# Performance work log

Hardware: AMD Instinct MI355X
Metric: run time of the kernel (lower is better)

The kernel has to match this reference:

```python
import jax, jax.numpy as jnp
import numpy as np

B, S, M = 8, 2048, 256
D = 512          # input/memory feature dim
P = 512          # proj_dim
H = 8            # num_heads


def setup_inputs() -> dict:
    key = jax.random.key(0)
    ks = jax.random.split(key, 10)
    sc = 0.02
    return {
        "input_seq": jax.random.normal(ks[0], (B, S, D), jnp.float32),
        "memory_cells": jax.random.normal(ks[1], (B, M, D), jnp.float32),
        "Wk": jax.random.normal(ks[2], (D, P), jnp.float32) * sc,
        "bk": jnp.zeros((P,), jnp.float32),
        "Wv": jax.random.normal(ks[3], (D, P), jnp.float32) * sc,
        "bv": jnp.zeros((P,), jnp.float32),
        "Wq": jax.random.normal(ks[4], (H, D, P), jnp.float32) * sc,  # stacked per-head query Dense
        "bq": jnp.zeros((H, P), jnp.float32),
        "Wo": jax.random.normal(ks[5], (H * P, P), jnp.float32) * sc,
        "bo": jnp.zeros((P,), jnp.float32),
    }


def reference(input_seq, memory_cells, Wk, bk, Wv, bv, Wq, bq, Wo, bo):
    # shared key/value projections (multi-query: one K/V for all heads)
    ik = input_seq @ Wk + bk          # [B,S,P]
    mk = memory_cells @ Wk + bk       # [B,M,P]
    iv = input_seq @ Wv + bv          # [B,S,P]
    mv = memory_cells @ Wv + bv       # [B,M,P]

    # per-head queries from memory cells, all heads at once
    q = jnp.einsum('bmd,hdp->bhmp', memory_cells, Wq) + bq[None, :, None, :]  # [B,H,M,P]

    input_score = jnp.einsum('bhmp,bsp->bhms', q, ik)          # [B,H,M,S]
    self_score = jnp.sum(q * mk[:, None], axis=-1, keepdims=True)  # [B,H,M,1]
    score = jnp.concatenate([self_score, input_score], axis=-1)    # [B,H,M,S+1]
    score = score / jnp.sqrt(jnp.float32(P))
    attn = jax.nn.softmax(score, axis=-1)

    self_attn = attn[..., 0:1]                                  # [B,H,M,1]
    input_attn = attn[..., 1:]                                  # [B,H,M,S]
    val = jnp.einsum('bhms,bsp->bhmp', input_attn, iv) + self_attn * mv[:, None]

    # concat heads: [B,M,H*P]
    concat = jnp.transpose(val, (0, 2, 1, 3)).reshape(B, M, H * P)
    return concat @ Wo + bo           # [B,M,P]
```

## Files before the change

kernel.cpp:

```cpp
#include <hip/hip_runtime.h>

#define B_ 8
#define S_ 2048
#define M_ 256
#define D_ 512
#define P_ 512
#define H_ 8

#define SCALE 0.044194173824159216f

typedef __attribute__((ext_vector_type(8))) short bf16x8;
typedef __attribute__((ext_vector_type(4))) float f32x4;

static __device__ __forceinline__ float bf2f(short u) {
  union { float f; unsigned int i; } x;
  x.i = ((unsigned int)(unsigned short)u) << 16;
  return x.f;
}
static __device__ __forceinline__ short f2bf(float f) {
  union { float f; unsigned int i; } x;
  x.f = f;
  unsigned int r = (x.i + 0x7FFFu + ((x.i >> 16) & 1u)) >> 16;
  return (short)r;
}

static __device__ __forceinline__ void gll16(const short* g, short* l) {
  __builtin_amdgcn_global_load_lds(
      (const __attribute__((address_space(1))) void*)g,
      (__attribute__((address_space(3))) void*)l, 16, 0, 0);
}

#define LGKM_WAIT() asm volatile("s_waitcnt lgkmcnt(0)" ::: "memory")
#define RAW_BAR() do { asm volatile("" ::: "memory"); __builtin_amdgcn_s_barrier(); asm volatile("" ::: "memory"); } while (0)

__global__ __launch_bounds__(256) void cast_both(
    const float* __restrict__ inA, short* __restrict__ outA, int n4A,
    const float* __restrict__ inM, short* __restrict__ outM)
{
  int idx = blockIdx.x * 256 + threadIdx.x;
  const float* in = inA;
  short* out = outA;
  if (idx >= n4A) { idx -= n4A; in = inM; out = outM; }
  float4 v = ((const float4*)in)[idx];
  short o0 = f2bf(v.x), o1 = f2bf(v.y), o2 = f2bf(v.z), o3 = f2bf(v.w);
  uint2 pk;
  pk.x = (unsigned int)(unsigned short)o0 | ((unsigned int)(unsigned short)o1 << 16);
  pk.y = (unsigned int)(unsigned short)o2 | ((unsigned int)(unsigned short)o3 << 16);
  ((uint2*)out)[idx] = pk;
}

__global__ __launch_bounds__(256) void wtrans_all(
    const float* __restrict__ Wk, const float* __restrict__ Wv,
    const float* __restrict__ Wq,
    short* __restrict__ WkT, short* __restrict__ WvT, short* __restrict__ WqT)
{
  __shared__ float tile[32][33];
  const int t = threadIdx.x, tx = t & 31, ty = t >> 5;
  const int z = blockIdx.z;
  const float* inp;
  short* outp;
  if (z == 0)      { inp = Wk; outp = WkT; }
  else if (z == 1) { inp = Wv; outp = WvT; }
  else             { inp = Wq + (size_t)(z - 2) * 512 * 512;
                     outp = WqT + (size_t)(z - 2) * 512 * 512; }
  const int n0 = blockIdx.x * 32, k0 = blockIdx.y * 32;
#pragma unroll
  for (int i = 0; i < 4; ++i)
    tile[ty + 8 * i][tx] = inp[(size_t)(k0 + ty + 8 * i) * 512 + n0 + tx];
  __syncthreads();
#pragma unroll
  for (int i = 0; i < 4; ++i)
    outp[(size_t)(n0 + ty + 8 * i) * 512 + k0 + tx] = f2bf(tile[tx][ty + 8 * i]);
}

__global__ __launch_bounds__(256) void wtrans_wo(
    const float* __restrict__ in, short* __restrict__ out)
{
  __shared__ float tile[32][33];
  const int t = threadIdx.x, tx = t & 31, ty = t >> 5;
  const int n0 = blockIdx.x * 32, k0 = blockIdx.y * 32;
#pragma unroll
  for (int i = 0; i < 4; ++i)
    tile[ty + 8 * i][tx] = in[(size_t)(k0 + ty + 8 * i) * 512 + n0 + tx];
  __syncthreads();
#pragma unroll
  for (int i = 0; i < 4; ++i)
    out[(size_t)(n0 + ty + 8 * i) * 4096 + k0 + tx] = f2bf(tile[tx][ty + 8 * i]);
}

template<int MODE, int K, int N, int LDA, int LDB>
__global__ __launch_bounds__(256, 3) void gemm128(
    const short* __restrict__ Abase, const short* __restrict__ Bbase,
    const float* __restrict__ bias, void* __restrict__ Cv,
    const size_t aZ, const size_t bZ, const size_t cZ,
    float* __restrict__ Ls,
    const float* __restrict__ eselfp, const short* __restrict__ mvbp)
{
  __shared__ short As[4096];
  __shared__ short Bs[4096];
  const int t = threadIdx.x;
  const int w = t >> 6, lane = t & 63, qd = lane >> 4, ln = lane & 15;
  const int wm = (w & 1) * 64, wn = (w >> 1) * 64;

  int z, m0, n0, bsel;
  if constexpr (MODE == 2 || MODE == 3) {
    const int b = blockIdx.x;
    n0 = blockIdx.y * 128;
    const int h = blockIdx.z & 7, mb = blockIdx.z >> 3;
    z = b * 8 + h;
    m0 = mb * 128;
    bsel = b;
  } else {
    n0 = blockIdx.x * 128;
    m0 = blockIdx.y * 128;
    z = blockIdx.z;
    bsel = z;
  }

  const short* A  = Abase + (size_t)z * aZ;
  const short* Bp = Bbase + (size_t)bsel * bZ;

  const int rr = t >> 2, g0 = t & 3;
  const int gs0 = g0 ^ ((rr >> 1) & 3);
  const int gs1 = g0 ^ (((rr + 64) >> 1) & 3);
  const short* ga0 = A + (size_t)(m0 + rr) * LDA + gs0 * 8;
  const short* ga1 = A + (size_t)(m0 + rr + 64) * LDA + gs1 * 8;
  const short* gb0 = Bp + (size_t)(n0 + rr) * LDB + gs0 * 8;
  const short* gb1 = Bp + (size_t)(n0 + rr + 64) * LDB + gs1 * 8;

  int aoff[4], boff[4];
#pragma unroll
  for (int mt = 0; mt < 4; ++mt) {
    int r = wm + mt * 16 + ln;
    aoff[mt] = r * 32 + (qd ^ ((r >> 1) & 3)) * 8;
  }
#pragma unroll
  for (int nt = 0; nt < 4; ++nt) {
    int r = wn + nt * 16 + ln;
    boff[nt] = r * 32 + (qd ^ ((r >> 1) & 3)) * 8;
  }

  f32x4 acc[4][4];
#pragma unroll
  for (int mt = 0; mt < 4; ++mt)
#pragma unroll
    for (int nt = 0; nt < 4; ++nt) acc[mt][nt] = (f32x4){0.f, 0.f, 0.f, 0.f};

  for (int kc = 0; kc < K; kc += 32) {
    __syncthreads();
    gll16(ga0 + kc, &As[w * 512]);
    gll16(ga1 + kc, &As[2048 + w * 512]);
    gll16(gb0 + kc, &Bs[w * 512]);
    gll16(gb1 + kc, &Bs[2048 + w * 512]);
    __syncthreads();

    bf16x8 af[4], bfr[4];
#pragma unroll
    for (int mt = 0; mt < 4; ++mt) af[mt] = *(const bf16x8*)&As[aoff[mt]];
#pragma unroll
    for (int nt = 0; nt < 4; ++nt) bfr[nt] = *(const bf16x8*)&Bs[boff[nt]];
#pragma unroll
    for (int mt = 0; mt < 4; ++mt)
#pragma unroll
      for (int nt = 0; nt < 4; ++nt)
        acc[mt][nt] = __builtin_amdgcn_mfma_f32_16x16x32_bf16(af[mt], bfr[nt], acc[mt][nt], 0, 0, 0);
  }

  if constexpr (MODE == 5) {
#pragma unroll
    for (int nt = 0; nt < 4; ++nt) {
      const int col = n0 + wn + nt * 16 + ln;
#pragma unroll
      for (int mt = 0; mt < 4; ++mt)
#pragma unroll
        for (int r = 0; r < 4; ++r) {
          const int row = m0 + wm + mt * 16 + qd * 4 + r;
          ((float*)Cv)[(size_t)z * cZ + (size_t)row * N + col] = acc[mt][nt][r];
        }
    }
  } else if constexpr (MODE == 2) {
#pragma unroll
    for (int mt = 0; mt < 4; ++mt)
#pragma unroll
      for (int nt = 0; nt < 4; ++nt)
#pragma unroll
        for (int r = 0; r < 4; ++r)
          acc[mt][nt][r] = __expf(acc[mt][nt][r] * SCALE);
#pragma unroll
    for (int mt = 0; mt < 4; ++mt)
#pragma unroll
      for (int r = 0; r < 4; ++r) {
        float rsum = acc[mt][0][r] + acc[mt][1][r] + acc[mt][2][r] + acc[mt][3][r];
        rsum += __shfl_xor(rsum, 1);
        rsum += __shfl_xor(rsum, 2);
        rsum += __shfl_xor(rsum, 4);
        rsum += __shfl_xor(rsum, 8);
        if (ln == 0) {
          const int row = m0 + wm + mt * 16 + qd * 4 + r;
          atomicAdd(&Ls[(size_t)z * M_ + row], rsum);
        }
      }
#pragma unroll
    for (int nt = 0; nt < 4; ++nt) {
      const int col = n0 + wn + nt * 16 + ln;
#pragma unroll
      for (int mt = 0; mt < 4; ++mt)
#pragma unroll
        for (int r = 0; r < 4; ++r) {
          const int row = m0 + wm + mt * 16 + qd * 4 + r;
          ((short*)Cv)[(size_t)z * cZ + (size_t)row * N + col] = f2bf(acc[mt][nt][r]);
        }
    }
  } else if constexpr (MODE == 3) {
    const int zb = z >> 3, hh = z & 7;
#pragma unroll
    for (int mt = 0; mt < 4; ++mt)
#pragma unroll
      for (int r = 0; r < 4; ++r) {
        const int row = m0 + wm + mt * 16 + qd * 4 + r;
        const float es = eselfp[(size_t)z * M_ + row];
        const float inv = 1.f / (es + Ls[(size_t)z * M_ + row]);
        const short* mvr = mvbp + ((size_t)(zb * M_ + row)) * P_;
        short* outr = (short*)Cv + ((size_t)(zb * M_ + row)) * (H_ * P_) + (size_t)hh * P_;
#pragma unroll
        for (int nt = 0; nt < 4; ++nt) {
          const int col = n0 + wn + nt * 16 + ln;
          outr[col] = f2bf((acc[mt][nt][r] + es * bf2f(mvr[col])) * inv);
        }
      }
  } else {
#pragma unroll
    for (int nt = 0; nt < 4; ++nt) {
      const int col = n0 + wn + nt * 16 + ln;
      const float bc = bias[512 * z + col];
#pragma unroll
      for (int mt = 0; mt < 4; ++mt)
#pragma unroll
        for (int r = 0; r < 4; ++r) {
          const int row = m0 + wm + mt * 16 + qd * 4 + r;
          const int bidx = row >> 8, ml = row & 255;
          ((short*)Cv)[((size_t)(bidx * H_ + z) * M_ + ml) * N + col] = f2bf(acc[mt][nt][r] + bc);
        }
    }
  }
}

template<int MH, int NH>
static __device__ __forceinline__ void mfma_quad(
    f32x4 (&acc)[8][4], const bf16x8 (&a)[4][2], const bf16x8 (&bfr)[2][2])
{
  __builtin_amdgcn_s_setprio(1);
#pragma unroll
  for (int kk = 0; kk < 2; ++kk)
#pragma unroll
    for (int mt = 0; mt < 4; ++mt)
#pragma unroll
      for (int nt = 0; nt < 2; ++nt)
        acc[MH * 4 + mt][NH * 2 + nt] = __builtin_amdgcn_mfma_f32_16x16x32_bf16(
            a[mt][kk], bfr[nt][kk], acc[MH * 4 + mt][NH * 2 + nt], 0, 0, 0);
  __builtin_amdgcn_s_setprio(0);
}

template<int MODE, int K, int LDA, int LDB>
__global__ __launch_bounds__(512, 2) void gemm256(
    const short* __restrict__ Abase, const short* __restrict__ Bbase,
    void* __restrict__ Cv, float* __restrict__ Ls,
    const float* __restrict__ eselfp, const short* __restrict__ mvbp,
    const size_t aZ, const size_t bZ)
{
  __shared__ short lds[65536];
  constexpr int NKT = K / 64;
  static_assert(NKT >= 2, "need at least 2 K-tiles");
  const int t = threadIdx.x;
  const int w = t >> 6, lane = t & 63, qd = lane >> 4, ln = lane & 15;
  const int wr = w >> 2, wc = w & 3;
  const int b = blockIdx.x;
  const int n0 = blockIdx.y * 256, m0 = blockIdx.z * 256;

  const short* A  = Abase + (size_t)b * aZ;
  const short* Bp = Bbase + (size_t)b * bZ;

  const int s0 = w * 64 + lane, s1 = s0 + 512;
  const int sr0 = s0 >> 3, sc0 = ((s0 & 7) ^ (sr0 & 7)) * 8;
  const int sr1 = s1 >> 3, sc1 = ((s1 & 7) ^ (sr1 & 7)) * 8;

  auto stage = [&](const short* gorigin, int ldg, short* lbase) {
    gll16(gorigin + (size_t)sr0 * ldg + sc0, lbase + w * 512);
    gll16(gorigin + (size_t)sr1 * ldg + sc1, lbase + 4096 + w * 512);
  };

  const int cq0 = ((qd    ) ^ (ln & 7)) * 8;
  const int cq1 = ((4 + qd) ^ (ln & 7)) * 8;
  const int brow = (wc & 1) * 64;

  f32x4 acc[8][4];
#pragma unroll
  for (int i = 0; i < 8; ++i)
#pragma unroll
    for (int j = 0; j < 4; ++j) acc[i][j] = (f32x4){0.f, 0.f, 0.f, 0.f};

  stage(A  + (size_t)m0 * LDA,          LDA, &lds[0]);
  stage(A  + (size_t)(m0 + 128) * LDA,  LDA, &lds[8192]);
  stage(Bp + (size_t)n0 * LDB,          LDB, &lds[32768]);
  stage(Bp + (size_t)(n0 + 128) * LDB,  LDB, &lds[32768 + 8192]);
  stage(Bp + (size_t)n0 * LDB + 64,     LDB, &lds[32768 + 16384]);
  asm volatile("s_waitcnt vmcnt(2)" ::: "memory");
  __builtin_amdgcn_s_barrier();

#pragma unroll 1
  for (int kt = 0; kt < NKT; ++kt) {
    const int p = kt & 1;
    short* Ah = &lds[p * 16384 + wr * 8192];
    short* Bh = &lds[32768 + p * 16384 + (wc >> 1) * 8192];
    bf16x8 a[4][2], bfr[2][2];

#pragma unroll
    for (int mt = 0; mt < 4; ++mt) {
      a[mt][0] = *(const bf16x8*)&Ah[(mt * 16 + ln) * 64 + cq0];
      a[mt][1] = *(const bf16x8*)&Ah[(mt * 16 + ln) * 64 + cq1];
    }
#pragma unroll
    for (int nt = 0; nt < 2; ++nt) {
      bfr[nt][0] = *(const bf16x8*)&Bh[(brow + nt * 16 + ln) * 64 + cq0];
      bfr[nt][1] = *(const bf16x8*)&Bh[(brow + nt * 16 + ln) * 64 + cq1];
    }
    if (kt + 1 < NKT) {
      stage(A  + (size_t)m0 * LDA + (kt + 1) * 64,          LDA, &lds[(p ^ 1) * 16384]);
      stage(Bp + (size_t)(n0 + 128) * LDB + (kt + 1) * 64,  LDB, &lds[32768 + (p ^ 1) * 16384 + 8192]);
    }
    RAW_BAR(); LGKM_WAIT();
    mfma_quad<0, 0>(acc, a, bfr);
    RAW_BAR();

#pragma unroll
    for (int mt = 0; mt < 4; ++mt) {
      a[mt][0] = *(const bf16x8*)&Ah[4096 + (mt * 16 + ln) * 64 + cq0];
      a[mt][1] = *(const bf16x8*)&Ah[4096 + (mt * 16 + ln) * 64 + cq1];
    }
    if (kt + 1 < NKT)
      stage(A + (size_t)(m0 + 128) * LDA + (kt + 1) * 64, LDA, &lds[(p ^ 1) * 16384 + 8192]);
    RAW_BAR(); LGKM_WAIT();
    mfma_quad<1, 0>(acc, a, bfr);
    RAW_BAR();

#pragma unroll
    for (int nt = 0; nt < 2; ++nt) {
      bfr[nt][0] = *(const bf16x8*)&Bh[(brow + 32 + nt * 16 + ln) * 64 + cq0];
      bfr[nt][1] = *(const bf16x8*)&Bh[(brow + 32 + nt * 16 + ln) * 64 + cq1];
    }
    RAW_BAR(); LGKM_WAIT();
    mfma_quad<1, 1>(acc, a, bfr);
    RAW_BAR();

#pragma unroll
    for (int mt = 0; mt < 4; ++mt) {
      a[mt][0] = *(const bf16x8*)&Ah[(mt * 16 + ln) * 64 + cq0];
      a[mt][1] = *(const bf16x8*)&Ah[(mt * 16 + ln) * 64 + cq1];
    }
    if (kt + 2 < NKT)
      stage(Bp + (size_t)n0 * LDB + (kt + 2) * 64, LDB, &lds[32768 + p * 16384]);
    RAW_BAR(); LGKM_WAIT();
    mfma_quad<0, 1>(acc, a, bfr);
    if (kt + 2 < NKT) { asm volatile("s_waitcnt vmcnt(2)" ::: "memory"); }
    else              { asm volatile("s_waitcnt vmcnt(0)" ::: "memory"); }
    RAW_BAR();
  }

  if constexpr (MODE == 2) {
#pragma unroll
    for (int i = 0; i < 8; ++i)
#pragma unroll
      for (int j = 0; j < 4; ++j)
#pragma unroll
        for (int r = 0; r < 4; ++r)
          acc[i][j][r] = __expf(acc[i][j][r] * SCALE);
#pragma unroll
    for (int i = 0; i < 8; ++i)
#pragma unroll
      for (int r = 0; r < 4; ++r) {
        float rs = acc[i][0][r] + acc[i][1][r] + acc[i][2][r] + acc[i][3][r];
        rs += __shfl_xor(rs, 1);
        rs += __shfl_xor(rs, 2);
        rs += __shfl_xor(rs, 4);
        rs += __shfl_xor(rs, 8);
        if (ln == 0) {
          const int row = m0 + wr * 128 + i * 16 + qd * 4 + r;
          atomicAdd(&Ls[(size_t)b * 2048 + row], rs);
        }
      }
    short* Cb = (short*)Cv + (size_t)b * 2048 * 2048;
#pragma unroll
    for (int j = 0; j < 4; ++j) {
      const int col = n0 + wc * 64 + j * 16 + ln;
#pragma unroll
      for (int i = 0; i < 8; ++i)
#pragma unroll
        for (int r = 0; r < 4; ++r) {
          const int row = m0 + wr * 128 + i * 16 + qd * 4 + r;
          Cb[(size_t)row * 2048 + col] = f2bf(acc[i][j][r]);
        }
    }
  } else {
#pragma unroll
    for (int i = 0; i < 8; ++i)
#pragma unroll
      for (int r = 0; r < 4; ++r) {
        const int R = m0 + wr * 128 + i * 16 + qd * 4 + r;
        const float es  = eselfp[(size_t)b * 2048 + R];
        const float inv = 1.f / (es + Ls[(size_t)b * 2048 + R]);
        const int h = R >> 8, m = R & 255;
        const short* mvr = mvbp + ((size_t)(b * 256 + m)) * 512;
        short* outr = (short*)Cv + ((size_t)(b * 256 + m)) * 4096 + (size_t)h * 512;
#pragma unroll
        for (int j = 0; j < 4; ++j) {
          const int col = n0 + wc * 64 + j * 16 + ln;
          outr[col] = f2bf((acc[i][j][r] + es * bf2f(mvr[col])) * inv);
        }
      }
  }
}

template<bool TRANSV>
__global__ __launch_bounds__(256, 3) void proj_kv(
    const short* __restrict__ A,
    const short* __restrict__ WkT, const short* __restrict__ WvT,
    const float* __restrict__ bk, const float* __restrict__ bv,
    short* __restrict__ Ck, short* __restrict__ Cvv)
{
  __shared__ short Sh[8192];
  short* As  = Sh;
  short* Bks = Sh + 4096;
  short* Bvs = Sh + 6144;
  const int t = threadIdx.x;
  const int w = t >> 6, lane = t & 63, qd = lane >> 4, ln = lane & 15;
  const int n0 = blockIdx.x * 64, m0 = blockIdx.y * 128;
  const int wm = (w & 1) * 64, wn2 = (w >> 1) * 32;

  const int rr = t >> 2, g0 = t & 3;
  const int gs0 = g0 ^ ((rr >> 1) & 3);
  const int gs1 = g0 ^ (((rr + 64) >> 1) & 3);
  const short* ga0 = A + (size_t)(m0 + rr) * 512 + gs0 * 8;
  const short* ga1 = A + (size_t)(m0 + rr + 64) * 512 + gs1 * 8;
  const short* gbk = WkT + (size_t)(n0 + rr) * 512 + gs0 * 8;
  const short* gbv = WvT + (size_t)(n0 + rr) * 512 + gs0 * 8;

  int aoff[4], boff[2];
#pragma unroll
  for (int mt = 0; mt < 4; ++mt) {
    int r = wm + mt * 16 + ln;
    aoff[mt] = r * 32 + (qd ^ ((r >> 1) & 3)) * 8;
  }
#pragma unroll
  for (int nt = 0; nt < 2; ++nt) {
    int r = wn2 + nt * 16 + ln;
    boff[nt] = r * 32 + (qd ^ ((r >> 1) & 3)) * 8;
  }

  f32x4 accK[4][2], accV[4][2];
#pragma unroll
  for (int mt = 0; mt < 4; ++mt)
#pragma unroll
    for (int nt = 0; nt < 2; ++nt) {
      accK[mt][nt] = (f32x4){0.f, 0.f, 0.f, 0.f};
      accV[mt][nt] = (f32x4){0.f, 0.f, 0.f, 0.f};
    }

  for (int kc = 0; kc < 512; kc += 32) {
    __syncthreads();
    gll16(ga0 + kc, &As[w * 512]);
    gll16(ga1 + kc, &As[2048 + w * 512]);
    gll16(gbk + kc, &Bks[w * 512]);
    gll16(gbv + kc, &Bvs[w * 512]);
    __syncthreads();

    bf16x8 af[4], bkf[2], bvf[2];
#pragma unroll
    for (int mt = 0; mt < 4; ++mt) af[mt] = *(const bf16x8*)&As[aoff[mt]];
#pragma unroll
    for (int nt = 0; nt < 2; ++nt) {
      bkf[nt] = *(const bf16x8*)&Bks[boff[nt]];
      bvf[nt] = *(const bf16x8*)&Bvs[boff[nt]];
    }
#pragma unroll
    for (int mt = 0; mt < 4; ++mt)
#pragma unroll
      for (int nt = 0; nt < 2; ++nt) {
        accK[mt][nt] = __builtin_amdgcn_mfma_f32_16x16x32_bf16(af[mt], bkf[nt], accK[mt][nt], 0, 0, 0);
        accV[mt][nt] = __builtin_amdgcn_mfma_f32_16x16x32_bf16(af[mt], bvf[nt], accV[mt][nt], 0, 0, 0);
      }
  }

#pragma unroll
  for (int nt = 0; nt < 2; ++nt) {
    const int col = n0 + wn2 + nt * 16 + ln;
    const float bc = bk[col];
#pragma unroll
    for (int mt = 0; mt < 4; ++mt)
#pragma unroll
      for (int r = 0; r < 4; ++r) {
        const int row = m0 + wm + mt * 16 + qd * 4 + r;
        Ck[(size_t)row * 512 + col] = f2bf(accK[mt][nt][r] + bc);
      }
  }

  if constexpr (!TRANSV) {
#pragma unroll
    for (int nt = 0; nt < 2; ++nt) {
      const int col = n0 + wn2 + nt * 16 + ln;
      const float bc = bv[col];
#pragma unroll
      for (int mt = 0; mt < 4; ++mt)
#pragma unroll
        for (int r = 0; r < 4; ++r) {
          const int row = m0 + wm + mt * 16 + qd * 4 + r;
          Cvv[(size_t)row * 512 + col] = f2bf(accV[mt][nt][r] + bc);
        }
    }
  } else {
    __syncthreads();
    short* ep = &Sh[w * 1280];
    const int lr = lane >> 1, lc16 = (lane & 1) * 16;
#pragma unroll
    for (int pass = 0; pass < 2; ++pass) {
#pragma unroll
      for (int mh = 0; mh < 2; ++mh) {
        const int mt = pass * 2 + mh;
#pragma unroll
        for (int nt = 0; nt < 2; ++nt) {
          const float bc = bv[n0 + wn2 + nt * 16 + ln];
#pragma unroll
          for (int r = 0; r < 4; ++r)
            ep[(nt * 16 + ln) * 40 + mh * 16 + qd * 4 + r] = f2bf(accV[mt][nt][r] + bc);
        }
      }
      LGKM_WAIT();
      const int srow0 = m0 + wm + pass * 32;
      const int bidx = srow0 >> 11;
      const int sloc = (srow0 & 2047) + lc16;
      const int pcol = n0 + wn2 + lr;
      short* outp = Cvv + (size_t)bidx * P_ * S_ + (size_t)pcol * S_ + sloc;
      *(bf16x8*)outp = *(const bf16x8*)&ep[lr * 40 + lc16];
      *(bf16x8*)(outp + 8) = *(const bf16x8*)&ep[lr * 40 + lc16 + 8];
      LGKM_WAIT();
    }
  }
}

__global__ __launch_bounds__(256) void reduce_wo(
    const float* __restrict__ partial, const float* __restrict__ bo,
    float* __restrict__ out)
{
  const int idx4 = blockIdx.x * 256 + threadIdx.x;
  float4 s = ((const float4*)bo)[idx4 & 127];
#pragma unroll
  for (int zz = 0; zz < 4; ++zz) {
    float4 p = ((const float4*)partial)[(size_t)zz * 262144 + idx4];
    s.x += p.x; s.y += p.y; s.z += p.z; s.w += p.w;
  }
  ((float4*)out)[idx4] = s;
}

__global__ __launch_bounds__(256) void selfscore(
    const short* __restrict__ qb, const short* __restrict__ mkb,
    float* __restrict__ eself, float* __restrict__ Ls)
{
  const int z = blockIdx.x, t = threadIdx.x;
  const short* qr = qb + ((size_t)z * M_ + t) * P_;
  const short* mr = mkb + ((size_t)(z >> 3) * M_ + t) * P_;
  float s = 0.f;
#pragma unroll 8
  for (int c = 0; c < P_; c += 8) {
    bf16x8 qv = *(const bf16x8*)(qr + c);
    bf16x8 mv = *(const bf16x8*)(mr + c);
#pragma unroll
    for (int j = 0; j < 8; ++j) s += bf2f(qv[j]) * bf2f(mv[j]);
  }
  eself[(size_t)z * M_ + t] = __expf(s * SCALE);
  Ls[(size_t)z * M_ + t] = 0.f;
}

extern "C" void kernel_launch(void* const* d_in, const int* in_sizes, int n_in,
                              void* d_out, int out_size, void* d_ws, size_t ws_size,
                              hipStream_t stream) {
  const float* input_seq = (const float*)d_in[0];
  const float* memcells  = (const float*)d_in[1];
  const float* Wk = (const float*)d_in[2];
  const float* bk = (const float*)d_in[3];
  const float* Wv = (const float*)d_in[4];
  const float* bv = (const float*)d_in[5];
  const float* Wq = (const float*)d_in[6];
  const float* bq = (const float*)d_in[7];
  const float* Wo = (const float*)d_in[8];
  const float* bo = (const float*)d_in[9];
  float* out = (float*)d_out;

  short* ws = (short*)d_ws;
  size_t o = 0;
  short* valb = ws + o; o += (size_t)B_ * M_ * H_ * P_;
  short* WoT  = ws + o; o += (size_t)(H_ * P_) * P_;
  short* mvb  = ws + o; o += (size_t)B_ * M_ * P_;
  short* mkb  = ws + o; o += (size_t)B_ * M_ * P_;
  short* qb   = ws + o; o += (size_t)B_ * H_ * M_ * P_;
  short* ivT  = ws + o; o += (size_t)B_ * P_ * S_;
  short* ikb  = ws + o; o += (size_t)B_ * S_ * P_;
  float* partial = (float*)(ws + o); o += (size_t)B_ * H_ * M_ * P_;
  float* eself = (float*)(ws + o); o += 2 * (size_t)B_ * H_ * M_;
  float* Ls    = (float*)(ws + o); o += 2 * (size_t)B_ * H_ * M_;
  short* region2 = ws + o;
  short* Ab  = region2;
  short* Mb  = Ab + (size_t)B_ * S_ * D_;
  short* WkT = Mb + (size_t)B_ * M_ * D_;
  short* WvT = WkT + (size_t)D_ * P_;
  short* WqT = WvT + (size_t)D_ * P_;
  short* Eb  = region2;

  dim3 blk(256);

  const int n4A = B_ * S_ * D_ / 4;
  const int n4M = B_ * M_ * D_ / 4;
  cast_both<<<dim3((n4A + n4M) / 256), blk, 0, stream>>>(input_seq, Ab, n4A, memcells, Mb);
  wtrans_all<<<dim3(16, 16, 10), blk, 0, stream>>>(Wk, Wv, Wq, WkT, WvT, WqT);
  wtrans_wo<<<dim3(16, 128), blk, 0, stream>>>(Wo, WoT);

  proj_kv<true><<<dim3(8, 128), blk, 0, stream>>>(Ab, WkT, WvT, bk, bv, ikb, ivT);
  proj_kv<false><<<dim3(8, 16), blk, 0, stream>>>(Mb, WkT, WvT, bk, bv, mkb, mvb);

  gemm128<1, 512, 512, 512, 512><<<dim3(4, 16, 8), blk, 0, stream>>>(
      Mb, WqT, bq, qb, 0, (size_t)D_ * P_, 0, nullptr, nullptr, nullptr);

  selfscore<<<dim3(64), blk, 0, stream>>>(qb, mkb, eself, Ls);

  gemm256<2, 512, 512, 512><<<dim3(8, 8, 8), dim3(512), 0, stream>>>(
      qb, ikb, Eb, Ls, nullptr, nullptr,
      (size_t)2048 * 512, (size_t)2048 * 512);

  gemm256<3, 2048, 2048, 2048><<<dim3(8, 2, 8), dim3(512), 0, stream>>>(
      Eb, ivT, valb, Ls, eself, mvb,
      (size_t)2048 * 2048, (size_t)512 * 2048);

  gemm128<5, 1024, 512, 4096, 4096><<<dim3(4, 16, 4), blk, 0, stream>>>(
      valb, WoT, nullptr, partial, 1024, 1024,
      (size_t)2048 * 512, nullptr, nullptr, nullptr);
  reduce_wo<<<dim3(1024), blk, 0, stream>>>(partial, bo, out);
}
```

Baseline: 325.3 us.

## Split attention GEMMs into qk256 and pv128 kernels with LDS-staged coalesced stores

Replaces the templated gemm256 with two kernels. qk256 reorders its global-to-LDS staging and MFMA phases, and writes the exp-score tile back through LDS so global stores are 16-byte and coalesced. pv128 narrows the N tile to 128, which doubles the grid from 128 to 256 blocks so the CUs fill better, and it also stages its normalized output through LDS for wide stores. It also drops the unused MODE 2/3 paths from gemm128 and adds a sched_barrier after the LDS waits. The cost is extra LDS traffic in the epilogues, and the narrower P·V tile reuses each A tile less.

```diff
diff --git a/kernel.cpp b/kernel.cpp
--- a/kernel.cpp
+++ b/kernel.cpp
@@ -31,6 +31,8 @@
 }
 
 #define LGKM_WAIT() asm volatile("s_waitcnt lgkmcnt(0)" ::: "memory")
+#define LGKM_SYNC() do { asm volatile("s_waitcnt lgkmcnt(0)" ::: "memory"); \
+                         __builtin_amdgcn_sched_barrier(0); } while (0)
 #define RAW_BAR() do { asm volatile("" ::: "memory"); __builtin_amdgcn_s_barrier(); asm volatile("" ::: "memory"); } while (0)
 
 __global__ __launch_bounds__(256) void cast_both(
@@ -102,20 +104,10 @@
   const int w = t >> 6, lane = t & 63, qd = lane >> 4, ln = lane & 15;
   const int wm = (w & 1) * 64, wn = (w >> 1) * 64;
 
-  int z, m0, n0, bsel;
-  if constexpr (MODE == 2 || MODE == 3) {
-    const int b = blockIdx.x;
-    n0 = blockIdx.y * 128;
-    const int h = blockIdx.z & 7, mb = blockIdx.z >> 3;
-    z = b * 8 + h;
-    m0 = mb * 128;
-    bsel = b;
-  } else {
-    n0 = blockIdx.x * 128;
-    m0 = blockIdx.y * 128;
-    z = blockIdx.z;
-    bsel = z;
-  }
+  const int n0 = blockIdx.x * 128;
+  const int m0 = blockIdx.y * 128;
+  const int z = blockIdx.z;
+  const int bsel = z;
 
   const short* A  = Abase + (size_t)z * aZ;
   const short* Bp = Bbase + (size_t)bsel * bZ;
@@ -178,56 +170,6 @@
           ((float*)Cv)[(size_t)z * cZ + (size_t)row * N + col] = acc[mt][nt][r];
         }
     }
-  } else if constexpr (MODE == 2) {
-#pragma unroll
-    for (int mt = 0; mt < 4; ++mt)
-#pragma unroll
-      for (int nt = 0; nt < 4; ++nt)
-#pragma unroll
-        for (int r = 0; r < 4; ++r)
-          acc[mt][nt][r] = __expf(acc[mt][nt][r] * SCALE);
-#pragma unroll
-    for (int mt = 0; mt < 4; ++mt)
-#pragma unroll
-      for (int r = 0; r < 4; ++r) {
-        float rsum = acc[mt][0][r] + acc[mt][1][r] + acc[mt][2][r] + acc[mt][3][r];
-        rsum += __shfl_xor(rsum, 1);
-        rsum += __shfl_xor(rsum, 2);
-        rsum += __shfl_xor(rsum, 4);
-        rsum += __shfl_xor(rsum, 8);
-        if (ln == 0) {
-          const int row = m0 + wm + mt * 16 + qd * 4 + r;
-          atomicAdd(&Ls[(size_t)z * M_ + row], rsum);
-        }
-      }
-#pragma unroll
-    for (int nt = 0; nt < 4; ++nt) {
-      const int col = n0 + wn + nt * 16 + ln;
-#pragma unroll
-      for (int mt = 0; mt < 4; ++mt)
-#pragma unroll
-        for (int r = 0; r < 4; ++r) {
-          const int row = m0 + wm + mt * 16 + qd * 4 + r;
-          ((short*)Cv)[(size_t)z * cZ + (size_t)row * N + col] = f2bf(acc[mt][nt][r]);
-        }
-    }
-  } else if constexpr (MODE == 3) {
-    const int zb = z >> 3, hh = z & 7;
-#pragma unroll
-    for (int mt = 0; mt < 4; ++mt)
-#pragma unroll
-      for (int r = 0; r < 4; ++r) {
-        const int row = m0 + wm + mt * 16 + qd * 4 + r;
-        const float es = eselfp[(size_t)z * M_ + row];
-        const float inv = 1.f / (es + Ls[(size_t)z * M_ + row]);
-        const short* mvr = mvbp + ((size_t)(zb * M_ + row)) * P_;
-        short* outr = (short*)Cv + ((size_t)(zb * M_ + row)) * (H_ * P_) + (size_t)hh * P_;
-#pragma unroll
-        for (int nt = 0; nt < 4; ++nt) {
-          const int col = n0 + wn + nt * 16 + ln;
-          outr[col] = f2bf((acc[mt][nt][r] + es * bf2f(mvr[col])) * inv);
-        }
-      }
   } else {
 #pragma unroll
     for (int nt = 0; nt < 4; ++nt) {
@@ -261,32 +203,41 @@
   __builtin_amdgcn_s_setprio(0);
 }
 
-template<int MODE, int K, int LDA, int LDB>
-__global__ __launch_bounds__(512, 2) void gemm256(
+template<int MH, int NT>
+static __device__ __forceinline__ void mfma_oct(
+    f32x4 (&acc)[8][2], const bf16x8 (&a)[4][2], const bf16x8 (&bv)[2])
+{
+  __builtin_amdgcn_s_setprio(1);
+#pragma unroll
+  for (int kk = 0; kk < 2; ++kk)
+#pragma unroll
+    for (int mt = 0; mt < 4; ++mt)
+      acc[MH * 4 + mt][NT] = __builtin_amdgcn_mfma_f32_16x16x32_bf16(
+          a[mt][kk], bv[kk], acc[MH * 4 + mt][NT], 0, 0, 0);
+  __builtin_amdgcn_s_setprio(0);
+}
+
+template<int NKT>
+__global__ __launch_bounds__(512, 2) void qk256(
     const short* __restrict__ Abase, const short* __restrict__ Bbase,
-    void* __restrict__ Cv, float* __restrict__ Ls,
-    const float* __restrict__ eselfp, const short* __restrict__ mvbp,
-    const size_t aZ, const size_t bZ)
+    short* __restrict__ Eb, float* __restrict__ Ls)
 {
   __shared__ short lds[65536];
-  constexpr int NKT = K / 64;
-  static_assert(NKT >= 2, "need at least 2 K-tiles");
   const int t = threadIdx.x;
   const int w = t >> 6, lane = t & 63, qd = lane >> 4, ln = lane & 15;
   const int wr = w >> 2, wc = w & 3;
   const int b = blockIdx.x;
   const int n0 = blockIdx.y * 256, m0 = blockIdx.z * 256;
 
-  const short* A  = Abase + (size_t)b * aZ;
-  const short* Bp = Bbase + (size_t)b * bZ;
+  const short* A  = Abase + (size_t)b * (2048 * 512) + (size_t)m0 * 512;
+  const short* Bp = Bbase + (size_t)b * (2048 * 512) + (size_t)n0 * 512;
 
   const int s0 = w * 64 + lane, s1 = s0 + 512;
   const int sr0 = s0 >> 3, sc0 = ((s0 & 7) ^ (sr0 & 7)) * 8;
   const int sr1 = s1 >> 3, sc1 = ((s1 & 7) ^ (sr1 & 7)) * 8;
-
-  auto stage = [&](const short* gorigin, int ldg, short* lbase) {
-    gll16(gorigin + (size_t)sr0 * ldg + sc0, lbase + w * 512);
-    gll16(gorigin + (size_t)sr1 * ldg + sc1, lbase + 4096 + w * 512);
+  auto stage = [&](const short* g, short* lbase) {
+    gll16(g + (size_t)sr0 * 512 + sc0, lbase + w * 512);
+    gll16(g + (size_t)sr1 * 512 + sc1, lbase + 4096 + w * 512);
   };
 
   const int cq0 = ((qd    ) ^ (ln & 7)) * 8;
@@ -299,12 +250,13 @@
 #pragma unroll
     for (int j = 0; j < 4; ++j) acc[i][j] = (f32x4){0.f, 0.f, 0.f, 0.f};
 
-  stage(A  + (size_t)m0 * LDA,          LDA, &lds[0]);
-  stage(A  + (size_t)(m0 + 128) * LDA,  LDA, &lds[8192]);
-  stage(Bp + (size_t)n0 * LDB,          LDB, &lds[32768]);
-  stage(Bp + (size_t)(n0 + 128) * LDB,  LDB, &lds[32768 + 8192]);
-  stage(Bp + (size_t)n0 * LDB + 64,     LDB, &lds[32768 + 16384]);
-  asm volatile("s_waitcnt vmcnt(2)" ::: "memory");
+  stage(A,                  &lds[0]);
+  stage(A + 128 * 512,      &lds[8192]);
+  stage(Bp,                 &lds[32768]);
+  stage(Bp + 128 * 512,     &lds[32768 + 8192]);
+  stage(A + 64,             &lds[16384]);
+  stage(A + 128 * 512 + 64, &lds[16384 + 8192]);
+  asm volatile("s_waitcnt vmcnt(4)" ::: "memory");
   __builtin_amdgcn_s_barrier();
 
 #pragma unroll 1
@@ -325,11 +277,20 @@
       bfr[nt][1] = *(const bf16x8*)&Bh[(brow + nt * 16 + ln) * 64 + cq1];
     }
     if (kt + 1 < NKT) {
-      stage(A  + (size_t)m0 * LDA + (kt + 1) * 64,          LDA, &lds[(p ^ 1) * 16384]);
-      stage(Bp + (size_t)(n0 + 128) * LDB + (kt + 1) * 64,  LDB, &lds[32768 + (p ^ 1) * 16384 + 8192]);
-    }
-    RAW_BAR(); LGKM_WAIT();
+      stage(Bp + (kt + 1) * 64,             &lds[32768 + (p ^ 1) * 16384]);
+      stage(Bp + 128 * 512 + (kt + 1) * 64, &lds[32768 + (p ^ 1) * 16384 + 8192]);
+    }
+    RAW_BAR(); LGKM_SYNC();
     mfma_quad<0, 0>(acc, a, bfr);
+    RAW_BAR();
+
+#pragma unroll
+    for (int nt = 0; nt < 2; ++nt) {
+      bfr[nt][0] = *(const bf16x8*)&Bh[(brow + 32 + nt * 16 + ln) * 64 + cq0];
+      bfr[nt][1] = *(const bf16x8*)&Bh[(brow + 32 + nt * 16 + ln) * 64 + cq1];
+    }
+    RAW_BAR(); LGKM_SYNC();
+    mfma_quad<0, 1>(acc, a, bfr);
     RAW_BAR();
 
 #pragma unroll
@@ -337,86 +298,184 @@
       a[mt][0] = *(const bf16x8*)&Ah[4096 + (mt * 16 + ln) * 64 + cq0];
       a[mt][1] = *(const bf16x8*)&Ah[4096 + (mt * 16 + ln) * 64 + cq1];
     }
-    if (kt + 1 < NKT)
-      stage(A + (size_t)(m0 + 128) * LDA + (kt + 1) * 64, LDA, &lds[(p ^ 1) * 16384 + 8192]);
-    RAW_BAR(); LGKM_WAIT();
-    mfma_quad<1, 0>(acc, a, bfr);
-    RAW_BAR();
-
-#pragma unroll
-    for (int nt = 0; nt < 2; ++nt) {
-      bfr[nt][0] = *(const bf16x8*)&Bh[(brow + 32 + nt * 16 + ln) * 64 + cq0];
-      bfr[nt][1] = *(const bf16x8*)&Bh[(brow + 32 + nt * 16 + ln) * 64 + cq1];
-    }
-    RAW_BAR(); LGKM_WAIT();
+    RAW_BAR(); LGKM_SYNC();
     mfma_quad<1, 1>(acc, a, bfr);
     RAW_BAR();
+
+#pragma unroll
+    for (int nt = 0; nt < 2; ++nt) {
+      bfr[nt][0] = *(const bf16x8*)&Bh[(brow + nt * 16 + ln) * 64 + cq0];
+      bfr[nt][1] = *(const bf16x8*)&Bh[(brow + nt * 16 + ln) * 64 + cq1];
+    }
+    if (kt + 2 < NKT) {
+      stage(A + (kt + 2) * 64,             &lds[p * 16384]);
+      stage(A + 128 * 512 + (kt + 2) * 64, &lds[p * 16384 + 8192]);
+    }
+    RAW_BAR(); LGKM_SYNC();
+    mfma_quad<1, 0>(acc, a, bfr);
+    if (kt + 2 < NKT) { asm volatile("s_waitcnt vmcnt(4)" ::: "memory"); }
+    else              { asm volatile("s_waitcnt vmcnt(0)" ::: "memory"); }
+    RAW_BAR();
+  }
+
+#pragma unroll
+  for (int i = 0; i < 8; ++i)
+#pragma unroll
+    for (int j = 0; j < 4; ++j)
+#pragma unroll
+      for (int r = 0; r < 4; ++r)
+        acc[i][j][r] = __expf(acc[i][j][r] * SCALE);
+#pragma unroll
+  for (int i = 0; i < 8; ++i)
+#pragma unroll
+    for (int r = 0; r < 4; ++r) {
+      float rs = acc[i][0][r] + acc[i][1][r] + acc[i][2][r] + acc[i][3][r];
+      rs += __shfl_xor(rs, 1);
+      rs += __shfl_xor(rs, 2);
+      rs += __shfl_xor(rs, 4);
+      rs += __shfl_xor(rs, 8);
+      if (ln == 0) {
+        const int row = m0 + wr * 128 + i * 16 + qd * 4 + r;
+        atomicAdd(&Ls[(size_t)b * 2048 + row], rs);
+      }
+    }
+#pragma unroll
+  for (int i = 0; i < 8; ++i)
+#pragma unroll
+    for (int j = 0; j < 4; ++j)
+#pragma unroll
+      for (int r = 0; r < 4; ++r) {
+        const int row = wr * 128 + i * 16 + qd * 4 + r;
+        const int col = wc * 64 + j * 16 + ln;
+        lds[row * 256 + (col ^ ((row & 7) << 3))] = f2bf(acc[i][j][r]);
+      }
+  LGKM_WAIT();
+  RAW_BAR();
+  short* Cb = Eb + (size_t)b * 2048 * 2048;
+#pragma unroll
+  for (int it = 0; it < 16; ++it) {
+    const int flat = it * 512 + t;
+    const int row = flat >> 5, c = flat & 31;
+    bf16x8 v = *(const bf16x8*)&lds[row * 256 + ((c ^ (row & 7)) * 8)];
+    *(bf16x8*)(Cb + (size_t)(m0 + row) * 2048 + n0 + c * 8) = v;
+  }
+}
+
+template<int NKT>
+__global__ __launch_bounds__(512, 2) void pv128(
+    const short* __restrict__ Abase, const short* __restrict__ Bbase,
+    short* __restrict__ valb, const float* __restrict__ Ls,
+    const float* __restrict__ eselfp, const short* __restrict__ mvbp)
+{
+  __shared__ short lds[49152];
+  const int t = threadIdx.x;
+  const int w = t >> 6, lane = t & 63, qd = lane >> 4, ln = lane & 15;
+  const int wr = w >> 2, wc = w & 3;
+  const int b = blockIdx.x;
+  const int n0 = blockIdx.y * 128;
+  const int bz = blockIdx.z;
+  const int m0 = bz * 256;
+
+  const short* A  = Abase + (size_t)b * (2048 * 2048) + (size_t)m0 * 2048;
+  const short* Bp = Bbase + (size_t)b * (512 * 2048) + (size_t)n0 * 2048;
+
+  const int s0 = w * 64 + lane, s1 = s0 + 512;
+  const int sr0 = s0 >> 3, sc0 = ((s0 & 7) ^ (sr0 & 7)) * 8;
+  const int sr1 = s1 >> 3, sc1 = ((s1 & 7) ^ (sr1 & 7)) * 8;
+  auto stage = [&](const short* g, short* lbase) {
+    gll16(g + (size_t)sr0 * 2048 + sc0, lbase + w * 512);
+    gll16(g + (size_t)sr1 * 2048 + sc1, lbase + 4096 + w * 512);
+  };
+
+  const int cq0 = ((qd    ) ^ (ln & 7)) * 8;
+  const int cq1 = ((4 + qd) ^ (ln & 7)) * 8;
+  const int brow = wc * 32;
+
+  f32x4 acc[8][2];
+#pragma unroll
+  for (int i = 0; i < 8; ++i)
+#pragma unroll
+    for (int j = 0; j < 2; ++j) acc[i][j] = (f32x4){0.f, 0.f, 0.f, 0.f};
+
+  stage(A,                   &lds[0]);
+  stage(A + 128 * 2048,      &lds[8192]);
+  stage(Bp,                  &lds[32768]);
+  stage(A + 64,              &lds[16384]);
+  stage(A + 128 * 2048 + 64, &lds[16384 + 8192]);
+  asm volatile("s_waitcnt vmcnt(4)" ::: "memory");
+  __builtin_amdgcn_s_barrier();
+
+#pragma unroll 1
+  for (int kt = 0; kt < NKT; ++kt) {
+    const int p = kt & 1;
+    short* Ah = &lds[p * 16384 + wr * 8192];
+    short* Bh = &lds[32768 + p * 8192];
+    bf16x8 a[4][2], bv[2];
 
 #pragma unroll
     for (int mt = 0; mt < 4; ++mt) {
       a[mt][0] = *(const bf16x8*)&Ah[(mt * 16 + ln) * 64 + cq0];
       a[mt][1] = *(const bf16x8*)&Ah[(mt * 16 + ln) * 64 + cq1];
     }
-    if (kt + 2 < NKT)
-      stage(Bp + (size_t)n0 * LDB + (kt + 2) * 64, LDB, &lds[32768 + p * 16384]);
-    RAW_BAR(); LGKM_WAIT();
-    mfma_quad<0, 1>(acc, a, bfr);
-    if (kt + 2 < NKT) { asm volatile("s_waitcnt vmcnt(2)" ::: "memory"); }
+    bv[0] = *(const bf16x8*)&Bh[(brow + ln) * 64 + cq0];
+    bv[1] = *(const bf16x8*)&Bh[(brow + ln) * 64 + cq1];
+    if (kt + 1 < NKT)
+      stage(Bp + (kt + 1) * 64, &lds[32768 + (p ^ 1) * 8192]);
+    RAW_BAR(); LGKM_SYNC();
+    mfma_oct<0, 0>(acc, a, bv);
+    RAW_BAR();
+
+    bv[0] = *(const bf16x8*)&Bh[(brow + 16 + ln) * 64 + cq0];
+    bv[1] = *(const bf16x8*)&Bh[(brow + 16 + ln) * 64 + cq1];
+    RAW_BAR(); LGKM_SYNC();
+    mfma_oct<0, 1>(acc, a, bv);
+    RAW_BAR();
+
+#pragma unroll
+    for (int mt = 0; mt < 4; ++mt) {
+      a[mt][0] = *(const bf16x8*)&Ah[4096 + (mt * 16 + ln) * 64 + cq0];
+      a[mt][1] = *(const bf16x8*)&Ah[4096 + (mt * 16 + ln) * 64 + cq1];
+    }
+    RAW_BAR(); LGKM_SYNC();
+    mfma_oct<1, 1>(acc, a, bv);
+    RAW_BAR();
+
+    bv[0] = *(const bf16x8*)&Bh[(brow + ln) * 64 + cq0];
+    bv[1] = *(const bf16x8*)&Bh[(brow + ln) * 64 + cq1];
+    if (kt + 2 < NKT) {
+      stage(A + (kt + 2) * 64,              &lds[p * 16384]);
+      stage(A + 128 * 2048 + (kt + 2) * 64, &lds[p * 16384 + 8192]);
+    }
+    RAW_BAR(); LGKM_SYNC();
+    mfma_oct<1, 0>(acc, a, bv);
+    if (kt + 2 < NKT) { asm volatile("s_waitcnt vmcnt(4)" ::: "memory"); }
     else              { asm volatile("s_waitcnt vmcnt(0)" ::: "memory"); }
     RAW_BAR();
   }
 
-  if constexpr (MODE == 2) {
-#pragma unroll
-    for (int i = 0; i < 8; ++i)
-#pragma unroll
-      for (int j = 0; j < 4; ++j)
-#pragma unroll
-        for (int r = 0; r < 4; ++r)
-          acc[i][j][r] = __expf(acc[i][j][r] * SCALE);
-#pragma unroll
-    for (int i = 0; i < 8; ++i)
-#pragma unroll
-      for (int r = 0; r < 4; ++r) {
-        float rs = acc[i][0][r] + acc[i][1][r] + acc[i][2][r] + acc[i][3][r];
-        rs += __shfl_xor(rs, 1);
-        rs += __shfl_xor(rs, 2);
-        rs += __shfl_xor(rs, 4);
-        rs += __shfl_xor(rs, 8);
-        if (ln == 0) {
-          const int row = m0 + wr * 128 + i * 16 + qd * 4 + r;
-          atomicAdd(&Ls[(size_t)b * 2048 + row], rs);
-        }
+#pragma unroll
+  for (int i = 0; i < 8; ++i)
+#pragma unroll
+    for (int r = 0; r < 4; ++r) {
+      const int row = wr * 128 + i * 16 + qd * 4 + r;
+      const float es  = eselfp[(size_t)b * 2048 + m0 + row];
+      const float inv = 1.f / (es + Ls[(size_t)b * 2048 + m0 + row]);
+      const short* mvr = mvbp + ((size_t)(b * 256 + row)) * 512;
+#pragma unroll
+      for (int j = 0; j < 2; ++j) {
+        const int lcol = wc * 32 + j * 16 + ln;
+        const float v = (acc[i][j][r] + es * bf2f(mvr[n0 + lcol])) * inv;
+        lds[row * 128 + (lcol ^ ((row & 7) << 3))] = f2bf(v);
       }
-    short* Cb = (short*)Cv + (size_t)b * 2048 * 2048;
-#pragma unroll
-    for (int j = 0; j < 4; ++j) {
-      const int col = n0 + wc * 64 + j * 16 + ln;
-#pragma unroll
-      for (int i = 0; i < 8; ++i)
-#pragma unroll
-        for (int r = 0; r < 4; ++r) {
-          const int row = m0 + wr * 128 + i * 16 + qd * 4 + r;
-          Cb[(size_t)row * 2048 + col] = f2bf(acc[i][j][r]);
-        }
-    }
-  } else {
-#pragma unroll
-    for (int i = 0; i < 8; ++i)
-#pragma unroll
-      for (int r = 0; r < 4; ++r) {
-        const int R = m0 + wr * 128 + i * 16 + qd * 4 + r;
-        const float es  = eselfp[(size_t)b * 2048 + R];
-        const float inv = 1.f / (es + Ls[(size_t)b * 2048 + R]);
-        const int h = R >> 8, m = R & 255;
-        const short* mvr = mvbp + ((size_t)(b * 256 + m)) * 512;
-        short* outr = (short*)Cv + ((size_t)(b * 256 + m)) * 4096 + (size_t)h * 512;
-#pragma unroll
-        for (int j = 0; j < 4; ++j) {
-          const int col = n0 + wc * 64 + j * 16 + ln;
-          outr[col] = f2bf((acc[i][j][r] + es * bf2f(mvr[col])) * inv);
-        }
-      }
+    }
+  LGKM_WAIT();
+  RAW_BAR();
+#pragma unroll
+  for (int it = 0; it < 8; ++it) {
+    const int flat = it * 512 + t;
+    const int row = flat >> 4, c = flat & 15;
+    bf16x8 v = *(const bf16x8*)&lds[row * 128 + ((c ^ (row & 7)) * 8)];
+    *(bf16x8*)(valb + ((size_t)(b * 256 + row)) * 4096 + (size_t)bz * 512 + n0 + c * 8) = v;
   }
 }
 
@@ -630,13 +689,9 @@
 
   selfscore<<<dim3(64), blk, 0, stream>>>(qb, mkb, eself, Ls);
 
-  gemm256<2, 512, 512, 512><<<dim3(8, 8, 8), dim3(512), 0, stream>>>(
-      qb, ikb, Eb, Ls, nullptr, nullptr,
-      (size_t)2048 * 512, (size_t)2048 * 512);
-
-  gemm256<3, 2048, 2048, 2048><<<dim3(8, 2, 8), dim3(512), 0, stream>>>(
-      Eb, ivT, valb, Ls, eself, mvb,
-      (size_t)2048 * 2048, (size_t)512 * 2048);
+  qk256<8><<<dim3(8, 8, 8), dim3(512), 0, stream>>>(qb, ikb, Eb, Ls);
+
+  pv128<32><<<dim3(8, 4, 8), dim3(512), 0, stream>>>(Eb, ivT, valb, Ls, eself, mvb);
 
   gemm128<5, 1024, 512, 4096, 4096><<<dim3(4, 16, 4), blk, 0, stream>>>(
       valb, WoT, nullptr, partial, 1024, 1024,
```

New measurement: 305.1 us. 1.07x faster.
